# Kernel tuning notes

Measured on AMD Instinct MI355X. Metric: run time of the kernel, lower is better.

The kernel has to match this reference:

```python
import jax, jax.numpy as jnp
import numpy as np

DIM = 1024
NUM_HEADS = 16
HEAD_DIM = DIM // NUM_HEADS
WINDOW = 1024
GATE_IN = 20
B, T = 2, 2048
ROPE_BASE = 10000.0


def setup_inputs() -> dict:
    key = jax.random.key(0)
    ks = jax.random.split(key, 12)
    s = 0.02
    x = jax.random.normal(ks[0], (B, T, DIM), dtype=jnp.float32)
    Wq = jax.random.normal(ks[1], (DIM, DIM), dtype=jnp.float32) * s
    bq = jnp.zeros((DIM,), jnp.float32)
    Wk = jax.random.normal(ks[2], (DIM, DIM), dtype=jnp.float32) * s
    bk = jnp.zeros((DIM,), jnp.float32)
    Wv = jax.random.normal(ks[3], (DIM, DIM), dtype=jnp.float32) * s
    bv = jnp.zeros((DIM,), jnp.float32)
    # o_lin.weight is zero-initialized in the original; use random here so the
    # reference output/grads are non-degenerate.
    Wo = jax.random.normal(ks[4], (DIM, DIM), dtype=jnp.float32) * s
    bo = jnp.zeros((DIM,), jnp.float32)
    Wg = jax.random.normal(ks[5], (NUM_HEADS, GATE_IN), dtype=jnp.float32) * s
    bg = jnp.zeros((NUM_HEADS,), jnp.float32)
    # rotary tables, half-dim convention
    inv_freq = 1.0 / (ROPE_BASE ** (jnp.arange(0, HEAD_DIM, 2, dtype=jnp.float32) / HEAD_DIM))
    t = jnp.arange(T, dtype=jnp.float32)
    freqs = jnp.outer(t, inv_freq)  # [T, HEAD_DIM/2]
    return {"x": x, "Wq": Wq, "bq": bq, "Wk": Wk, "bk": bk, "Wv": Wv, "bv": bv,
            "Wo": Wo, "bo": bo, "Wg": Wg, "bg": bg,
            "cos": jnp.cos(freqs), "sin": jnp.sin(freqs)}


def _rope(u, cos, sin):
    # u: [B,T,H,hd]; cos/sin: [T, hd/2]
    u1, u2 = jnp.split(u, 2, axis=-1)
    c = cos[None, :, None, :]
    s = sin[None, :, None, :]
    return jnp.concatenate([u1 * c - u2 * s, u1 * s + u2 * c], axis=-1)


def reference(x, Wq, bq, Wk, bk, Wv, bv, Wo, bo, Wg, bg, cos, sin):
    Bx, Tx, D = x.shape
    q = (x @ Wq.T + bq).reshape(Bx, Tx, NUM_HEADS, HEAD_DIM)
    k = (x @ Wk.T + bk).reshape(Bx, Tx, NUM_HEADS, HEAD_DIM)
    v = (x @ Wv.T + bv).reshape(Bx, Tx, NUM_HEADS, HEAD_DIM)
    q = _rope(q, cos, sin)
    k = _rope(k, cos, sin)
    scale = 1.0 / jnp.sqrt(jnp.float32(HEAD_DIM))
    scores = jnp.einsum('bqhd,bkhd->bhqk', q, k) * scale  # [B,H,T,T]
    i = jnp.arange(Tx)[:, None]
    j = jnp.arange(Tx)[None, :]
    mask = (j <= i) & (j >= i - WINDOW)  # causal + sliding window (WINDOW left, 0 right)
    scores = jnp.where(mask[None, None], scores, jnp.float32(-1e30))
    probs = jax.nn.softmax(scores, axis=-1)
    o = jnp.einsum('bhqk,bkhd->bqhd', probs, v)  # [B,T,H,hd]
    gate = jax.nn.sigmoid(x[..., :GATE_IN] @ Wg.T + bg)  # [B,T,H]
    o = o * gate[..., None]
    o = o.reshape(Bx, Tx, D)
    return o @ Wo.T + bo
```

## Files before the change

kernel.cpp:

```cpp
#include <hip/hip_runtime.h>

#define DIMM 1024
#define NHEADS 16
#define HDIM 64
#define WIN 1024
#define GATEIN 20
#define BB 2
#define TT 2048
#define MTOT (BB*TT)

typedef __attribute__((ext_vector_type(8))) short short8;
typedef __attribute__((ext_vector_type(4))) float f32x4;
typedef __attribute__((ext_vector_type(16))) float f32x16;
typedef const __attribute__((address_space(1))) void gvoid_t;
typedef __attribute__((address_space(3))) void lvoid_t;

__device__ __forceinline__ unsigned short f2b(float f) {
  union { float f; unsigned u; } c; c.f = f;
  unsigned u = c.u + 0x7fffu + ((c.u >> 16) & 1u);
  return (unsigned short)(u >> 16);
}
__device__ __forceinline__ float b2f(unsigned short s) {
  union { unsigned u; float f; } c; c.u = ((unsigned)s) << 16;
  return c.f;
}
__device__ __forceinline__ unsigned cvt_pk_bf16(float lo, float hi) {
  unsigned r;
  asm("v_cvt_pk_bf16_f32 %0, %1, %2" : "=v"(r) : "v"(lo), "v"(hi));
  return r;
}
__device__ __forceinline__ float max3f(float a, float b, float c) {
  return fmaxf(fmaxf(a, b), c);
}
__device__ __forceinline__ float xmax32(float x) {
  union { float f; unsigned u; } c; c.f = x;
  auto pr = __builtin_amdgcn_permlane32_swap(c.u, c.u, false, false);
  union { unsigned u; float f; } a, b; a.u = pr[0]; b.u = pr[1];
  return fmaxf(a.f, b.f);
}
__device__ __forceinline__ float xsum32(float x) {
  union { float f; unsigned u; } c; c.f = x;
  auto pr = __builtin_amdgcn_permlane32_swap(c.u, c.u, false, false);
  union { unsigned u; float f; } a, b; a.u = pr[0]; b.u = pr[1];
  return a.f + b.f;
}

__global__ void prep_kernel(const float* __restrict__ x,  const float* __restrict__ Wq,
                            const float* __restrict__ Wk, const float* __restrict__ Wv,
                            const float* __restrict__ Wo, const float* __restrict__ bq,
                            const float* __restrict__ bk, const float* __restrict__ bv,
                            unsigned short* __restrict__ xb, unsigned short* __restrict__ wqkv,
                            unsigned short* __restrict__ wob, float* __restrict__ bcat) {
  int i = blockIdx.x * blockDim.x + threadIdx.x;
  const float* src; unsigned short* dst; int off;
  if (i < 1048576)      { src = x;  dst = xb;             off = i; }
  else if (i < 1310720) { src = Wq; dst = wqkv;           off = i - 1048576; }
  else if (i < 1572864) { src = Wk; dst = wqkv + 1048576; off = i - 1310720; }
  else if (i < 1835008) { src = Wv; dst = wqkv + 2097152; off = i - 1572864; }
  else if (i < 2097152) { src = Wo; dst = wob;            off = i - 1835008; }
  else {
    int j = i - 2097152;
    if (j < 768) {
      const float* bsrc = (j < 256) ? bq : (j < 512) ? bk : bv;
      int bo = (j & 255) * 4;
      int db = (j < 256) ? 0 : (j < 512) ? 1024 : 2048;
      *(float4*)(bcat + db + bo) = *(const float4*)(bsrc + bo);
    }
    return;
  }
  float4 v = ((const float4*)src)[off];
  union { unsigned short s[4]; uint2 u; } o;
  o.s[0] = f2b(v.x); o.s[1] = f2b(v.y); o.s[2] = f2b(v.z); o.s[3] = f2b(v.w);
  *(uint2*)(dst + (size_t)off * 4) = o.u;
}

__global__ void gate_kernel(const float* __restrict__ x, const float* __restrict__ Wg,
                            const float* __restrict__ bg, float* __restrict__ gate) {
  int i = blockIdx.x * blockDim.x + threadIdx.x;
  if (i >= MTOT * NHEADS) return;
  int h = i & 15;
  int m = i >> 4;
  const float* xr = x + (size_t)m * DIMM;
  const float* wr = Wg + h * GATEIN;
  float z = bg[h];
#pragma unroll
  for (int g = 0; g < GATEIN; ++g) z += xr[g] * wr[g];
  gate[i] = 1.f / (1.f + __expf(-z));
}

template<int MF, int OUTBF>
__global__ __launch_bounds__(256) void gemm_bt(const unsigned short* __restrict__ A,
                                               const unsigned short* __restrict__ Bw,
                                               const float* __restrict__ bias,
                                               void* __restrict__ Cout,
                                               int M, int N, int K) {
  __shared__ __align__(16) unsigned short As[2][MF * 32 * 32];
  __shared__ __align__(16) unsigned short Bs[2][128 * 32];
  const int tid = threadIdx.x;
  const int lane = tid & 63, wid = tid >> 6;
  const int g = lane >> 4, r16 = lane & 15;
  const int m0 = blockIdx.y * (MF * 32), n0 = blockIdx.x * 128;
  const int wr = (wid >> 1) * (MF * 16), wc = (wid & 1) * 64;
  const int wbase = wid * 64;

  int oaf[MF], obf[4];
#pragma unroll
  for (int mf = 0; mf < MF; ++mf) {
    int row = wr + mf * 16 + r16;
    oaf[mf] = row * 32 + ((g ^ ((row >> 1) & 3)) * 8);
  }
#pragma unroll
  for (int nf = 0; nf < 4; ++nf) {
    int row = wc + nf * 16 + r16;
    obf[nf] = row * 32 + ((g ^ ((row >> 1) & 3)) * 8);
  }

  f32x4 acc[MF][4];
#pragma unroll
  for (int i = 0; i < MF; ++i)
#pragma unroll
    for (int j = 0; j < 4; ++j) acc[i][j] = (f32x4){0.f, 0.f, 0.f, 0.f};

  auto stage = [&](int buf, int k0) {
#pragma unroll
    for (int j = 0; j < MF / 2; ++j) {
      int sbase = j * 256 + wbase;
      int s = sbase + lane;
      int l = s ^ ((s >> 3) & 3);
      const unsigned short* gA = A + (size_t)(m0 + (l >> 2)) * K + k0 + (l & 3) * 8;
      __builtin_amdgcn_global_load_lds((gvoid_t*)gA,
          (lvoid_t*)((char*)&As[buf][0] + sbase * 16), 16, 0, 0);
    }
#pragma unroll
    for (int j = 0; j < 2; ++j) {
      int sbase = j * 256 + wbase;
      int s = sbase + lane;
      int l = s ^ ((s >> 3) & 3);
      const unsigned short* gB = Bw + (size_t)(n0 + (l >> 2)) * K + k0 + (l & 3) * 8;
      __builtin_amdgcn_global_load_lds((gvoid_t*)gB,
          (lvoid_t*)((char*)&Bs[buf][0] + sbase * 16), 16, 0, 0);
    }
  };

  const int NT = K >> 5;
  stage(0, 0);
  __syncthreads();
  for (int t = 0; t < NT; ++t) {
    const int buf = t & 1;
    if (t + 1 < NT) stage(buf ^ 1, (t + 1) << 5);
    short8 af[MF], bf[4];
#pragma unroll
    for (int mf = 0; mf < MF; ++mf) af[mf] = *(const short8*)(&As[buf][0] + oaf[mf]);
#pragma unroll
    for (int nf = 0; nf < 4; ++nf)  bf[nf] = *(const short8*)(&Bs[buf][0] + obf[nf]);
#pragma unroll
    for (int mf = 0; mf < MF; ++mf)
#pragma unroll
      for (int nf = 0; nf < 4; ++nf)
        acc[mf][nf] = __builtin_amdgcn_mfma_f32_16x16x32_bf16(af[mf], bf[nf], acc[mf][nf], 0, 0, 0);
    __syncthreads();
  }
#pragma unroll
  for (int mf = 0; mf < MF; ++mf)
#pragma unroll
    for (int nf = 0; nf < 4; ++nf)
#pragma unroll
      for (int rr = 0; rr < 4; ++rr) {
        int m = m0 + wr + mf * 16 + g * 4 + rr;
        int n = n0 + wc + nf * 16 + r16;
        float v = acc[mf][nf][rr] + bias[n];
        if (OUTBF) ((unsigned short*)Cout)[(size_t)m * N + n] = f2b(v);
        else       ((float*)Cout)[(size_t)m * N + n] = v;
      }
}

#define QSCALE (0.125f * 1.4426950408889634f)
__global__ __launch_bounds__(256) void ropev_kernel(const unsigned short* __restrict__ qkv,
                                                    const float* __restrict__ cosb,
                                                    const float* __restrict__ sinb,
                                                    unsigned short* __restrict__ qr,
                                                    unsigned short* __restrict__ kr,
                                                    unsigned short* __restrict__ vt) {
  __shared__ unsigned short tile[64][66];
  const int t0 = blockIdx.x * 64;
  const int bh = blockIdx.y;
  const int b = bh >> 4, h = bh & 15;
  const int tid = threadIdx.x;
  const int tr = tid >> 2;
  const int qd = tid & 3;
  const int t = t0 + tr;
  const size_t base = (size_t)bh * TT * HDIM;
  const unsigned short* row = qkv + (size_t)(b * TT + t) * 3072 + h * 64;

  {
    const unsigned short* vsrc = row + 2048 + qd * 16;
    short8 v0 = *(const short8*)vsrc;
    short8 v1 = *(const short8*)(vsrc + 8);
#pragma unroll
    for (int j = 0; j < 8; ++j) {
      tile[tr][qd * 16 + j]     = (unsigned short)v0[j];
      tile[tr][qd * 16 + 8 + j] = (unsigned short)v1[j];
    }
  }

  {
    const int d0 = qd * 8;
    short8 q1 = *(const short8*)(row + d0);
    short8 q2 = *(const short8*)(row + d0 + 32);
    short8 k1 = *(const short8*)(row + 1024 + d0);
    short8 k2 = *(const short8*)(row + 1024 + d0 + 32);
    float4 c0 = *(const float4*)(cosb + t * 32 + d0);
    float4 c1 = *(const float4*)(cosb + t * 32 + d0 + 4);
    float4 s0 = *(const float4*)(sinb + t * 32 + d0);
    float4 s1 = *(const float4*)(sinb + t * 32 + d0 + 4);
    float cc[8] = {c0.x, c0.y, c0.z, c0.w, c1.x, c1.y, c1.z, c1.w};
    float ss[8] = {s0.x, s0.y, s0.z, s0.w, s1.x, s1.y, s1.z, s1.w};
    short8 qo1, qo2, ko1, ko2;
#pragma unroll
    for (int j = 0; j < 8; ++j) {
      float a1 = b2f((unsigned short)q1[j]), a2 = b2f((unsigned short)q2[j]);
      float b1 = b2f((unsigned short)k1[j]), b2v = b2f((unsigned short)k2[j]);
      qo1[j] = (short)f2b((a1 * cc[j] - a2 * ss[j]) * QSCALE);
      qo2[j] = (short)f2b((a1 * ss[j] + a2 * cc[j]) * QSCALE);
      ko1[j] = (short)f2b(b1 * cc[j] - b2v * ss[j]);
      ko2[j] = (short)f2b(b1 * ss[j] + b2v * cc[j]);
    }
    *(short8*)(qr + base + (size_t)t * HDIM + d0)      = qo1;
    *(short8*)(qr + base + (size_t)t * HDIM + d0 + 32) = qo2;
    size_t ok = base + (size_t)(t >> 5) * 2048 + (size_t)(qd >> 1) * 512
              + (size_t)(qd & 1) * 256 + (size_t)(t & 31) * 8;
    *(short8*)(kr + ok)        = ko1;
    *(short8*)(kr + ok + 1024) = ko2;
  }
  __syncthreads();

  {
    const int d = tid >> 2;
    const int tc = (tid & 3) * 16;
    short8 o0, o1;
#pragma unroll
    for (int j = 0; j < 8; ++j) {
      o0[j] = (short)tile[tc + j][d];
      o1[j] = (short)tile[tc + 8 + j][d];
    }
    int kt = (t0 + tc) >> 5;
    int n  = (tc >> 4) & 1;
    int m  = d >> 5, l31v = d & 31;
    size_t A0 = base + (size_t)kt * 2048 + (size_t)(m * 2 + n) * 512 + (size_t)l31v * 8;
    *(short8*)(vt + A0)       = o0;
    *(short8*)(vt + A0 + 256) = o1;
  }
}

__global__ __launch_bounds__(256, 4) void attn_kernel(const unsigned short* __restrict__ qr,
                                                      const unsigned short* __restrict__ kr,
                                                      const unsigned short* __restrict__ vt,
                                                      const float* __restrict__ gate,
                                                      unsigned short* __restrict__ attn_out) {
  __shared__ float lds_m[4][32];
  __shared__ float lds_l[4][32];
  __shared__ float lds_O[3][64][33];
  const int tid = threadIdx.x;
  const int lane = tid & 63, wid = tid >> 6;
  const int l31 = lane & 31, hi = lane >> 5;

  const int fid = blockIdx.x;
  const int idx = fid >> 3;
  const int bh = (fid & 7) * 4 + (idx & 3);
  const int qt = 63 - (idx >> 2);
  const int q0 = qt * 32;
  const int b = bh >> 4, h = bh & 15;
  const unsigned short* kptr = kr + (size_t)bh * TT * HDIM;
  const unsigned short* vptr = vt + (size_t)bh * TT * HDIM;
  const int q = q0 + l31;

  short8 qf[4];
#pragma unroll
  for (int st = 0; st < 4; ++st)
    qf[st] = *(const short8*)(qr + (size_t)bh * TT * HDIM + (size_t)q * HDIM + st * 16 + hi * 8);

  f32x16 o0, o1;
#pragma unroll
  for (int r = 0; r < 16; ++r) { o0[r] = 0.f; o1[r] = 0.f; }
  float mrun = -1e30f, lrun = 0.f;

  int kv_lo = q0 - WIN;
  if (kv_lo < 0) kv_lo = 0;
  const int kv_hi = q0 + 32;

  for (int kv = kv_lo + wid * 32; kv < kv_hi; kv += 128) {
    const unsigned short* kf = kptr + (size_t)kv * 64 + lane * 8;
    short8 k0 = *(const short8*)(kf);
    short8 k1 = *(const short8*)(kf + 512);
    short8 k2 = *(const short8*)(kf + 1024);
    short8 k3 = *(const short8*)(kf + 1536);

    f32x16 s;
#pragma unroll
    for (int r = 0; r < 16; ++r) s[r] = 0.f;
    s = __builtin_amdgcn_mfma_f32_32x32x16_bf16(k0, qf[0], s, 0, 0, 0);
    s = __builtin_amdgcn_mfma_f32_32x32x16_bf16(k1, qf[1], s, 0, 0, 0);
    s = __builtin_amdgcn_mfma_f32_32x32x16_bf16(k2, qf[2], s, 0, 0, 0);
    s = __builtin_amdgcn_mfma_f32_32x32x16_bf16(k3, qf[3], s, 0, 0, 0);

    if (kv == q0) {
#pragma unroll
      for (int r = 0; r < 16; ++r) {
        int key = kv + (r & 3) + 8 * (r >> 2) + 4 * hi;
        s[r] = (key <= q) ? s[r] : -1e30f;
      }
    } else if (q0 >= WIN && kv == kv_lo) {
#pragma unroll
      for (int r = 0; r < 16; ++r) {
        int key = kv + (r & 3) + 8 * (r >> 2) + 4 * hi;
        s[r] = (key + WIN >= q) ? s[r] : -1e30f;
      }
    }

    float t0 = max3f(s[0],  s[1],  s[2]);
    float t1 = max3f(s[3],  s[4],  s[5]);
    float t2 = max3f(s[6],  s[7],  s[8]);
    float t3 = max3f(s[9],  s[10], s[11]);
    float t4 = max3f(s[12], s[13], s[14]);
    float lm = fmaxf(max3f(t0, t1, t2), max3f(t3, t4, s[15]));
    lm = xmax32(lm);

    if (!__all(lm - mrun <= 8.f)) {
      float mnew = fmaxf(mrun, lm);
      float scf = __builtin_exp2f(mrun - mnew);
      mrun = mnew;
      lrun *= scf;
#pragma unroll
      for (int r = 0; r < 16; ++r) { o0[r] *= scf; o1[r] *= scf; }
    }

#pragma unroll
    for (int r = 0; r < 16; ++r) s[r] = __builtin_exp2f(s[r] - mrun);

    float c0 = (s[0] + s[1]) + (s[2] + s[3]);
    float c1 = (s[4] + s[5]) + (s[6] + s[7]);
    float c2 = (s[8] + s[9]) + (s[10] + s[11]);
    float c3 = (s[12] + s[13]) + (s[14] + s[15]);
    lrun += xsum32((c0 + c1) + (c2 + c3));

    unsigned w0 = cvt_pk_bf16(s[0],  s[1]),  w1 = cvt_pk_bf16(s[2],  s[3]);
    unsigned w2 = cvt_pk_bf16(s[4],  s[5]),  w3 = cvt_pk_bf16(s[6],  s[7]);
    unsigned w4 = cvt_pk_bf16(s[8],  s[9]),  w5 = cvt_pk_bf16(s[10], s[11]);
    unsigned w6 = cvt_pk_bf16(s[12], s[13]), w7 = cvt_pk_bf16(s[14], s[15]);
    auto s1p = __builtin_amdgcn_permlane32_swap(w0, w2, false, false);
    auto s2p = __builtin_amdgcn_permlane32_swap(w1, w3, false, false);
    auto s3p = __builtin_amdgcn_permlane32_swap(w4, w6, false, false);
    auto s4p = __builtin_amdgcn_permlane32_swap(w5, w7, false, false);
    union { unsigned u[4]; short8 s8; } pf0, pf1;
    pf0.u[0] = s1p[0]; pf0.u[1] = s2p[0]; pf0.u[2] = s1p[1]; pf0.u[3] = s2p[1];
    pf1.u[0] = s3p[0]; pf1.u[1] = s4p[0]; pf1.u[2] = s3p[1]; pf1.u[3] = s4p[1];

    const unsigned short* vf = vptr + (size_t)kv * 64 + lane * 8;
    short8 vf00 = *(const short8*)(vf);
    short8 vf01 = *(const short8*)(vf + 512);
    short8 vf10 = *(const short8*)(vf + 1024);
    short8 vf11 = *(const short8*)(vf + 1536);

    o0 = __builtin_amdgcn_mfma_f32_32x32x16_bf16(vf00, pf0.s8, o0, 0, 0, 0);
    o1 = __builtin_amdgcn_mfma_f32_32x32x16_bf16(vf10, pf0.s8, o1, 0, 0, 0);
    o0 = __builtin_amdgcn_mfma_f32_32x32x16_bf16(vf01, pf1.s8, o0, 0, 0, 0);
    o1 = __builtin_amdgcn_mfma_f32_32x32x16_bf16(vf11, pf1.s8, o1, 0, 0, 0);
  }

  if (hi == 0) { lds_m[wid][l31] = mrun; lds_l[wid][l31] = lrun; }
  __syncthreads();
  float m0 = lds_m[0][l31], m1 = lds_m[1][l31], m2 = lds_m[2][l31], m3 = lds_m[3][l31];
  float mstar = fmaxf(fmaxf(m0, m1), fmaxf(m2, m3));
  float myscale = __builtin_exp2f(mrun - mstar);
  if (wid != 0) {
#pragma unroll
    for (int r = 0; r < 16; ++r) {
      lds_O[wid - 1][lane][r]      = o0[r] * myscale;
      lds_O[wid - 1][lane][16 + r] = o1[r] * myscale;
    }
  }
  __syncthreads();
  if (wid == 0) {
    float lstar = __builtin_exp2f(m0 - mstar) * lds_l[0][l31]
                + __builtin_exp2f(m1 - mstar) * lds_l[1][l31]
                + __builtin_exp2f(m2 - mstar) * lds_l[2][l31]
                + __builtin_exp2f(m3 - mstar) * lds_l[3][l31];
    float gv = gate[((size_t)b * TT + q) * NHEADS + h];
    float inv = gv / lstar;
    float of0[16], of1[16];
#pragma unroll
    for (int r = 0; r < 16; ++r) {
      of0[r] = o0[r] * myscale + lds_O[0][lane][r]      + lds_O[1][lane][r]      + lds_O[2][lane][r];
      of1[r] = o1[r] * myscale + lds_O[0][lane][16 + r] + lds_O[1][lane][16 + r] + lds_O[2][lane][16 + r];
    }
    unsigned short* orow = attn_out + ((size_t)b * TT + q) * DIMM + h * HDIM;
#pragma unroll
    for (int a2 = 0; a2 < 4; ++a2) {
      int d0 = a2 * 8 + hi * 4;
      union { unsigned short s[4]; uint2 u; } x0, x1;
#pragma unroll
      for (int c = 0; c < 4; ++c) {
        x0.s[c] = f2b(of0[a2 * 4 + c] * inv);
        x1.s[c] = f2b(of1[a2 * 4 + c] * inv);
      }
      *(uint2*)(orow + d0) = x0.u;
      *(uint2*)(orow + 32 + d0) = x1.u;
    }
  }
}

#define OFF_XB    ((size_t)0)
#define OFF_WQKV  ((size_t)8388608)
#define OFF_WO    ((size_t)14680064)
#define OFF_BCAT  ((size_t)16777216)
#define OFF_QKV   ((size_t)16793600)
#define OFF_QR    ((size_t)41959424)
#define OFF_KR    ((size_t)50348032)
#define OFF_VT    ((size_t)58736640)
#define OFF_ATTN  ((size_t)67125248)
#define OFF_GATE  ((size_t)75513856)

extern "C" void kernel_launch(void* const* d_in, const int* in_sizes, int n_in,
                              void* d_out, int out_size, void* d_ws, size_t ws_size,
                              hipStream_t stream) {
  const float* x    = (const float*)d_in[0];
  const float* Wq   = (const float*)d_in[1];
  const float* bq   = (const float*)d_in[2];
  const float* Wk   = (const float*)d_in[3];
  const float* bk   = (const float*)d_in[4];
  const float* Wv   = (const float*)d_in[5];
  const float* bv   = (const float*)d_in[6];
  const float* Wo   = (const float*)d_in[7];
  const float* bo   = (const float*)d_in[8];
  const float* Wg   = (const float*)d_in[9];
  const float* bg   = (const float*)d_in[10];
  const float* cosb = (const float*)d_in[11];
  const float* sinb = (const float*)d_in[12];
  float* out = (float*)d_out;
  char* ws = (char*)d_ws;

  unsigned short* xb    = (unsigned short*)(ws + OFF_XB);
  unsigned short* wqkv  = (unsigned short*)(ws + OFF_WQKV);
  unsigned short* wob   = (unsigned short*)(ws + OFF_WO);
  float*          bcat  = (float*)(ws + OFF_BCAT);
  unsigned short* qkv   = (unsigned short*)(ws + OFF_QKV);
  unsigned short* q_r   = (unsigned short*)(ws + OFF_QR);
  unsigned short* k_r   = (unsigned short*)(ws + OFF_KR);
  unsigned short* v_t   = (unsigned short*)(ws + OFF_VT);
  unsigned short* attn  = (unsigned short*)(ws + OFF_ATTN);
  float*          gateb = (float*)(ws + OFF_GATE);

  prep_kernel<<<8195, 256, 0, stream>>>(x, Wq, Wk, Wv, Wo, bq, bk, bv, xb, wqkv, wob, bcat);
  gate_kernel<<<256, 256, 0, stream>>>(x, Wg, bg, gateb);

  gemm_bt<4, 1><<<dim3(24, 32), 256, 0, stream>>>(xb, wqkv, bcat, qkv, MTOT, 3072, 1024);

  ropev_kernel<<<dim3(32, 32), 256, 0, stream>>>(qkv, cosb, sinb, q_r, k_r, v_t);

  attn_kernel<<<2048, 256, 0, stream>>>(q_r, k_r, v_t, gateb, attn);

  gemm_bt<2, 0><<<dim3(8, 64), 256, 0, stream>>>(attn, wob, bo, out, MTOT, 1024, 1024);
}
```

Measured before the change: 107.4 us.

## Fuse RoPE, Q scaling and V transpose into the QKV GEMM epilogue

```diff
diff --git a/kernel.cpp b/kernel.cpp
--- a/kernel.cpp
+++ b/kernel.cpp
@@ -44,6 +44,8 @@
   union { unsigned u; float f; } a, b; a.u = pr[0]; b.u = pr[1];
   return a.f + b.f;
 }
+
+#define QSCALE (0.125f * 1.4426950408889634f)
 
 __global__ void prep_kernel(const float* __restrict__ x,  const float* __restrict__ Wq,
                             const float* __restrict__ Wk, const float* __restrict__ Wv,
@@ -88,11 +90,136 @@
   gate[i] = 1.f / (1.f + __expf(-z));
 }
 
-template<int MF, int OUTBF>
+__global__ __launch_bounds__(256) void gemm_qkv(const unsigned short* __restrict__ A,
+                                                const unsigned short* __restrict__ Bw,
+                                                const float* __restrict__ bias,
+                                                const float* __restrict__ cosb,
+                                                const float* __restrict__ sinb,
+                                                unsigned short* __restrict__ qr,
+                                                unsigned short* __restrict__ kr,
+                                                unsigned short* __restrict__ vt) {
+  const int M = MTOT, N = 3072, K = DIMM;
+  __shared__ __align__(16) unsigned short As[2][128 * 32];
+  __shared__ __align__(16) unsigned short Bs[2][128 * 32];
+  const int tid = threadIdx.x;
+  const int lane = tid & 63, wid = tid >> 6;
+  const int g = lane >> 4, r16 = lane & 15;
+  const int m0 = blockIdx.y * 128, n0 = blockIdx.x * 128;
+  const int wr = (wid >> 1) * 64, wc = (wid & 1) * 64;
+  const int wbase = wid * 64;
+
+  int oaf[4], obf[4];
+#pragma unroll
+  for (int mf = 0; mf < 4; ++mf) {
+    int row = wr + mf * 16 + r16;
+    oaf[mf] = row * 32 + ((g ^ ((row >> 1) & 3)) * 8);
+  }
+#pragma unroll
+  for (int nf = 0; nf < 4; ++nf) {
+    int row = wc + nf * 16 + r16;
+    obf[nf] = row * 32 + ((g ^ ((row >> 1) & 3)) * 8);
+  }
+
+  f32x4 acc[4][4];
+#pragma unroll
+  for (int i = 0; i < 4; ++i)
+#pragma unroll
+    for (int j = 0; j < 4; ++j) acc[i][j] = (f32x4){0.f, 0.f, 0.f, 0.f};
+
+  auto stage = [&](int buf, int k0) {
+#pragma unroll
+    for (int j = 0; j < 2; ++j) {
+      int sbase = j * 256 + wbase;
+      int s = sbase + lane;
+      int l = s ^ ((s >> 3) & 3);
+      const unsigned short* gA = A + (size_t)(m0 + (l >> 2)) * K + k0 + (l & 3) * 8;
+      __builtin_amdgcn_global_load_lds((gvoid_t*)gA,
+          (lvoid_t*)((char*)&As[buf][0] + sbase * 16), 16, 0, 0);
+      const unsigned short* gB = Bw + (size_t)(n0 + (l >> 2)) * K + k0 + (l & 3) * 8;
+      __builtin_amdgcn_global_load_lds((gvoid_t*)gB,
+          (lvoid_t*)((char*)&Bs[buf][0] + sbase * 16), 16, 0, 0);
+    }
+  };
+
+  const int NT = K >> 5;
+  stage(0, 0);
+  __syncthreads();
+  for (int t = 0; t < NT; ++t) {
+    const int buf = t & 1;
+    if (t + 1 < NT) stage(buf ^ 1, (t + 1) << 5);
+    short8 af[4], bf[4];
+#pragma unroll
+    for (int mf = 0; mf < 4; ++mf) af[mf] = *(const short8*)(&As[buf][0] + oaf[mf]);
+#pragma unroll
+    for (int nf = 0; nf < 4; ++nf)  bf[nf] = *(const short8*)(&Bs[buf][0] + obf[nf]);
+#pragma unroll
+    for (int mf = 0; mf < 4; ++mf)
+#pragma unroll
+      for (int nf = 0; nf < 4; ++nf)
+        acc[mf][nf] = __builtin_amdgcn_mfma_f32_16x16x32_bf16(af[mf], bf[nf], acc[mf][nf], 0, 0, 0);
+    __syncthreads();
+  }
+
+  const int ncol = n0 + wc;
+  const int seg  = ncol >> 10;
+  const int h    = (ncol >> 6) & 15;
+  const int bb   = m0 >> 11;
+  const int tb   = (m0 + wr) & 2047;
+  const size_t base = (size_t)(bb * NHEADS + h) * TT * HDIM;
+  float bias_v[4];
+#pragma unroll
+  for (int nf = 0; nf < 4; ++nf) bias_v[nf] = bias[ncol + nf * 16 + r16];
+
+  if (seg == 2) {
+#pragma unroll
+    for (int mf = 0; mf < 4; ++mf) {
+      int kvt = (tb >> 5) + (mf >> 1);
+#pragma unroll
+      for (int nf = 0; nf < 4; ++nf) {
+        union { unsigned short s4[4]; uint2 u; } w;
+#pragma unroll
+        for (int rr = 0; rr < 4; ++rr) w.s4[rr] = f2b(acc[mf][nf][rr] + bias_v[nf]);
+        size_t addr = base + (size_t)kvt * 2048
+                    + (size_t)((nf >> 1) * 2 + (mf & 1)) * 512
+                    + (size_t)(g >> 1) * 256
+                    + (size_t)((nf & 1) * 16 + r16) * 8 + 4 * (g & 1);
+        *(uint2*)(vt + addr) = w.u;
+      }
+    }
+  } else {
+#pragma unroll
+    for (int mf = 0; mf < 4; ++mf) {
+#pragma unroll
+      for (int rr = 0; rr < 4; ++rr) {
+        int t = tb + mf * 16 + g * 4 + rr;
+#pragma unroll
+        for (int nf = 0; nf < 2; ++nf) {
+          int d = nf * 16 + r16;
+          float c = cosb[t * 32 + d], s = sinb[t * 32 + d];
+          float v1 = acc[mf][nf][rr]     + bias_v[nf];
+          float v2 = acc[mf][nf + 2][rr] + bias_v[nf + 2];
+          float o1 = v1 * c - v2 * s;
+          float o2 = v1 * s + v2 * c;
+          if (seg == 0) {
+            qr[base + (size_t)t * HDIM + d]      = f2b(o1 * QSCALE);
+            qr[base + (size_t)t * HDIM + d + 32] = f2b(o2 * QSCALE);
+          } else {
+            size_t ok = base + (size_t)(t >> 5) * 2048 + (size_t)nf * 512
+                      + (size_t)(r16 >> 3) * 256 + (size_t)(t & 31) * 8 + (r16 & 7);
+            kr[ok]        = f2b(o1);
+            kr[ok + 1024] = f2b(o2);
+          }
+        }
+      }
+    }
+  }
+}
+
+template<int MF>
 __global__ __launch_bounds__(256) void gemm_bt(const unsigned short* __restrict__ A,
                                                const unsigned short* __restrict__ Bw,
                                                const float* __restrict__ bias,
-                                               void* __restrict__ Cout,
+                                               float* __restrict__ Cout,
                                                int M, int N, int K) {
   __shared__ __align__(16) unsigned short As[2][MF * 32 * 32];
   __shared__ __align__(16) unsigned short Bs[2][128 * 32];
@@ -168,88 +295,8 @@
       for (int rr = 0; rr < 4; ++rr) {
         int m = m0 + wr + mf * 16 + g * 4 + rr;
         int n = n0 + wc + nf * 16 + r16;
-        float v = acc[mf][nf][rr] + bias[n];
-        if (OUTBF) ((unsigned short*)Cout)[(size_t)m * N + n] = f2b(v);
-        else       ((float*)Cout)[(size_t)m * N + n] = v;
+        Cout[(size_t)m * N + n] = acc[mf][nf][rr] + bias[n];
       }
-}
-
-#define QSCALE (0.125f * 1.4426950408889634f)
-__global__ __launch_bounds__(256) void ropev_kernel(const unsigned short* __restrict__ qkv,
-                                                    const float* __restrict__ cosb,
-                                                    const float* __restrict__ sinb,
-                                                    unsigned short* __restrict__ qr,
-                                                    unsigned short* __restrict__ kr,
-                                                    unsigned short* __restrict__ vt) {
-  __shared__ unsigned short tile[64][66];
-  const int t0 = blockIdx.x * 64;
-  const int bh = blockIdx.y;
-  const int b = bh >> 4, h = bh & 15;
-  const int tid = threadIdx.x;
-  const int tr = tid >> 2;
-  const int qd = tid & 3;
-  const int t = t0 + tr;
-  const size_t base = (size_t)bh * TT * HDIM;
-  const unsigned short* row = qkv + (size_t)(b * TT + t) * 3072 + h * 64;
-
-  {
-    const unsigned short* vsrc = row + 2048 + qd * 16;
-    short8 v0 = *(const short8*)vsrc;
-    short8 v1 = *(const short8*)(vsrc + 8);
-#pragma unroll
-    for (int j = 0; j < 8; ++j) {
-      tile[tr][qd * 16 + j]     = (unsigned short)v0[j];
-      tile[tr][qd * 16 + 8 + j] = (unsigned short)v1[j];
-    }
-  }
-
-  {
-    const int d0 = qd * 8;
-    short8 q1 = *(const short8*)(row + d0);
-    short8 q2 = *(const short8*)(row + d0 + 32);
-    short8 k1 = *(const short8*)(row + 1024 + d0);
-    short8 k2 = *(const short8*)(row + 1024 + d0 + 32);
-    float4 c0 = *(const float4*)(cosb + t * 32 + d0);
-    float4 c1 = *(const float4*)(cosb + t * 32 + d0 + 4);
-    float4 s0 = *(const float4*)(sinb + t * 32 + d0);
-    float4 s1 = *(const float4*)(sinb + t * 32 + d0 + 4);
-    float cc[8] = {c0.x, c0.y, c0.z, c0.w, c1.x, c1.y, c1.z, c1.w};
-    float ss[8] = {s0.x, s0.y, s0.z, s0.w, s1.x, s1.y, s1.z, s1.w};
-    short8 qo1, qo2, ko1, ko2;
-#pragma unroll
-    for (int j = 0; j < 8; ++j) {
-      float a1 = b2f((unsigned short)q1[j]), a2 = b2f((unsigned short)q2[j]);
-      float b1 = b2f((unsigned short)k1[j]), b2v = b2f((unsigned short)k2[j]);
-      qo1[j] = (short)f2b((a1 * cc[j] - a2 * ss[j]) * QSCALE);
-      qo2[j] = (short)f2b((a1 * ss[j] + a2 * cc[j]) * QSCALE);
-      ko1[j] = (short)f2b(b1 * cc[j] - b2v * ss[j]);
-      ko2[j] = (short)f2b(b1 * ss[j] + b2v * cc[j]);
-    }
-    *(short8*)(qr + base + (size_t)t * HDIM + d0)      = qo1;
-    *(short8*)(qr + base + (size_t)t * HDIM + d0 + 32) = qo2;
-    size_t ok = base + (size_t)(t >> 5) * 2048 + (size_t)(qd >> 1) * 512
-              + (size_t)(qd & 1) * 256 + (size_t)(t & 31) * 8;
-    *(short8*)(kr + ok)        = ko1;
-    *(short8*)(kr + ok + 1024) = ko2;
-  }
-  __syncthreads();
-
-  {
-    const int d = tid >> 2;
-    const int tc = (tid & 3) * 16;
-    short8 o0, o1;
-#pragma unroll
-    for (int j = 0; j < 8; ++j) {
-      o0[j] = (short)tile[tc + j][d];
-      o1[j] = (short)tile[tc + 8 + j][d];
-    }
-    int kt = (t0 + tc) >> 5;
-    int n  = (tc >> 4) & 1;
-    int m  = d >> 5, l31v = d & 31;
-    size_t A0 = base + (size_t)kt * 2048 + (size_t)(m * 2 + n) * 512 + (size_t)l31v * 8;
-    *(short8*)(vt + A0)       = o0;
-    *(short8*)(vt + A0 + 256) = o1;
-  }
 }
 
 __global__ __launch_bounds__(256, 4) void attn_kernel(const unsigned short* __restrict__ qr,
@@ -413,7 +460,6 @@
 #define OFF_WQKV  ((size_t)8388608)
 #define OFF_WO    ((size_t)14680064)
 #define OFF_BCAT  ((size_t)16777216)
-#define OFF_QKV   ((size_t)16793600)
 #define OFF_QR    ((size_t)41959424)
 #define OFF_KR    ((size_t)50348032)
 #define OFF_VT    ((size_t)58736640)
@@ -443,7 +489,6 @@
   unsigned short* wqkv  = (unsigned short*)(ws + OFF_WQKV);
   unsigned short* wob   = (unsigned short*)(ws + OFF_WO);
   float*          bcat  = (float*)(ws + OFF_BCAT);
-  unsigned short* qkv   = (unsigned short*)(ws + OFF_QKV);
   unsigned short* q_r   = (unsigned short*)(ws + OFF_QR);
   unsigned short* k_r   = (unsigned short*)(ws + OFF_KR);
   unsigned short* v_t   = (unsigned short*)(ws + OFF_VT);
@@ -453,11 +498,9 @@
   prep_kernel<<<8195, 256, 0, stream>>>(x, Wq, Wk, Wv, Wo, bq, bk, bv, xb, wqkv, wob, bcat);
   gate_kernel<<<256, 256, 0, stream>>>(x, Wg, bg, gateb);
 
-  gemm_bt<4, 1><<<dim3(24, 32), 256, 0, stream>>>(xb, wqkv, bcat, qkv, MTOT, 3072, 1024);
-
-  ropev_kernel<<<dim3(32, 32), 256, 0, stream>>>(qkv, cosb, sinb, q_r, k_r, v_t);
+  gemm_qkv<<<dim3(24, 32), 256, 0, stream>>>(xb, wqkv, bcat, cosb, sinb, q_r, k_r, v_t);
 
   attn_kernel<<<2048, 256, 0, stream>>>(q_r, k_r, v_t, gateb, attn);
 
-  gemm_bt<2, 0><<<dim3(8, 64), 256, 0, stream>>>(attn, wob, bo, out, MTOT, 1024, 1024);
-}
+  gemm_bt<2><<<dim3(8, 64), 256, 0, stream>>>(attn, wob, bo, out, MTOT, 1024, 1024);
+}
```

Measured after the change: 106.6 us, median of 2. About the same (-0.8%).

## Replace QKV GEMM with 256x256-tile, 512-thread kernel and deeper prefetch

Applied to the files above, without the earlier changes.

```diff
diff --git a/kernel.cpp b/kernel.cpp
--- a/kernel.cpp
+++ b/kernel.cpp
@@ -44,6 +44,8 @@
   union { unsigned u; float f; } a, b; a.u = pr[0]; b.u = pr[1];
   return a.f + b.f;
 }
+
+#define QSCALE (0.125f * 1.4426950408889634f)
 
 __global__ void prep_kernel(const float* __restrict__ x,  const float* __restrict__ Wq,
                             const float* __restrict__ Wk, const float* __restrict__ Wv,
@@ -88,93 +90,98 @@
   gate[i] = 1.f / (1.f + __expf(-z));
 }
 
-template<int MF, int OUTBF>
-__global__ __launch_bounds__(256) void gemm_bt(const unsigned short* __restrict__ A,
-                                               const unsigned short* __restrict__ Bw,
-                                               const float* __restrict__ bias,
-                                               void* __restrict__ Cout,
-                                               int M, int N, int K) {
-  __shared__ __align__(16) unsigned short As[2][MF * 32 * 32];
-  __shared__ __align__(16) unsigned short Bs[2][128 * 32];
+__global__ __launch_bounds__(512, 2) void gemm_qkv_256(const unsigned short* __restrict__ A,
+                                                       const unsigned short* __restrict__ Bw,
+                                                       const float* __restrict__ bias,
+                                                       unsigned short* __restrict__ qkv) {
+  const int K = DIMM, N = 3072;
+  __shared__ __align__(16) unsigned short ldsA[2][16384];
+  __shared__ __align__(16) unsigned short ldsB[2][16384];
   const int tid = threadIdx.x;
   const int lane = tid & 63, wid = tid >> 6;
   const int g = lane >> 4, r16 = lane & 15;
-  const int m0 = blockIdx.y * (MF * 32), n0 = blockIdx.x * 128;
-  const int wr = (wid >> 1) * (MF * 16), wc = (wid & 1) * 64;
-  const int wbase = wid * 64;
-
-  int oaf[MF], obf[4];
-#pragma unroll
-  for (int mf = 0; mf < MF; ++mf) {
-    int row = wr + mf * 16 + r16;
-    oaf[mf] = row * 32 + ((g ^ ((row >> 1) & 3)) * 8);
-  }
-#pragma unroll
-  for (int nf = 0; nf < 4; ++nf) {
-    int row = wc + nf * 16 + r16;
-    obf[nf] = row * 32 + ((g ^ ((row >> 1) & 3)) * 8);
-  }
-
-  f32x4 acc[MF][4];
-#pragma unroll
-  for (int i = 0; i < MF; ++i)
+  const int wm = wid >> 2, wn = wid & 3;
+  const int m0 = blockIdx.y * 256, n0 = blockIdx.x * 256;
+
+  int aoff[8][2], boff[4][2];
+#pragma unroll
+  for (int fr = 0; fr < 8; ++fr)
+#pragma unroll
+    for (int ks = 0; ks < 2; ++ks) {
+      int lb = (wm * 128 + fr * 16 + r16) * 128 + ks * 64 + g * 16;
+      aoff[fr][ks] = lb ^ (((lb >> 9) & 1) << 5);
+    }
+#pragma unroll
+  for (int fc = 0; fc < 4; ++fc)
+#pragma unroll
+    for (int ks = 0; ks < 2; ++ks) {
+      int lb = (wn * 64 + fc * 16 + r16) * 128 + ks * 64 + g * 16;
+      boff[fc][ks] = lb ^ (((lb >> 9) & 1) << 5);
+    }
+
+  f32x4 acc[8][4];
+#pragma unroll
+  for (int i = 0; i < 8; ++i)
 #pragma unroll
     for (int j = 0; j < 4; ++j) acc[i][j] = (f32x4){0.f, 0.f, 0.f, 0.f};
 
-  auto stage = [&](int buf, int k0) {
-#pragma unroll
-    for (int j = 0; j < MF / 2; ++j) {
-      int sbase = j * 256 + wbase;
-      int s = sbase + lane;
-      int l = s ^ ((s >> 3) & 3);
-      const unsigned short* gA = A + (size_t)(m0 + (l >> 2)) * K + k0 + (l & 3) * 8;
+  auto stage = [&](int buf, int kt) {
+    const int k0 = kt * 64;
+#pragma unroll
+    for (int i = 0; i < 4; ++i) {
+      int s = i * 512 + tid;
+      int l = s ^ (((s >> 5) & 1) << 1);
+      const unsigned short* gA = A + (size_t)(m0 + (l >> 3)) * K + k0 + (l & 7) * 8;
       __builtin_amdgcn_global_load_lds((gvoid_t*)gA,
-          (lvoid_t*)((char*)&As[buf][0] + sbase * 16), 16, 0, 0);
-    }
-#pragma unroll
-    for (int j = 0; j < 2; ++j) {
-      int sbase = j * 256 + wbase;
-      int s = sbase + lane;
-      int l = s ^ ((s >> 3) & 3);
-      const unsigned short* gB = Bw + (size_t)(n0 + (l >> 2)) * K + k0 + (l & 3) * 8;
+          (lvoid_t*)((char*)&ldsA[buf][0] + s * 16), 16, 0, 0);
+      const unsigned short* gB = Bw + (size_t)(n0 + (l >> 3)) * K + k0 + (l & 7) * 8;
       __builtin_amdgcn_global_load_lds((gvoid_t*)gB,
-          (lvoid_t*)((char*)&Bs[buf][0] + sbase * 16), 16, 0, 0);
+          (lvoid_t*)((char*)&ldsB[buf][0] + s * 16), 16, 0, 0);
     }
   };
 
-  const int NT = K >> 5;
+  const int NT = K >> 6;
   stage(0, 0);
-  __syncthreads();
+  stage(1, 1);
   for (int t = 0; t < NT; ++t) {
     const int buf = t & 1;
-    if (t + 1 < NT) stage(buf ^ 1, (t + 1) << 5);
-    short8 af[MF], bf[4];
-#pragma unroll
-    for (int mf = 0; mf < MF; ++mf) af[mf] = *(const short8*)(&As[buf][0] + oaf[mf]);
-#pragma unroll
-    for (int nf = 0; nf < 4; ++nf)  bf[nf] = *(const short8*)(&Bs[buf][0] + obf[nf]);
-#pragma unroll
-    for (int mf = 0; mf < MF; ++mf)
-#pragma unroll
-      for (int nf = 0; nf < 4; ++nf)
-        acc[mf][nf] = __builtin_amdgcn_mfma_f32_16x16x32_bf16(af[mf], bf[nf], acc[mf][nf], 0, 0, 0);
-    __syncthreads();
-  }
-#pragma unroll
-  for (int mf = 0; mf < MF; ++mf)
-#pragma unroll
-    for (int nf = 0; nf < 4; ++nf)
+    if (t < NT - 1) asm volatile("s_waitcnt vmcnt(8)" ::: "memory");
+    else            asm volatile("s_waitcnt vmcnt(0)" ::: "memory");
+    __builtin_amdgcn_s_barrier();
+
+    const char* Ab = (const char*)&ldsA[buf][0];
+    const char* Bb = (const char*)&ldsB[buf][0];
+    __builtin_amdgcn_s_setprio(1);
+#pragma unroll
+    for (int ks = 0; ks < 2; ++ks) {
+      short8 af[8], bf[4];
+#pragma unroll
+      for (int fr = 0; fr < 8; ++fr) af[fr] = *(const short8*)(Ab + aoff[fr][ks]);
+#pragma unroll
+      for (int fc = 0; fc < 4; ++fc) bf[fc] = *(const short8*)(Bb + boff[fc][ks]);
+#pragma unroll
+      for (int fr = 0; fr < 8; ++fr)
+#pragma unroll
+        for (int fc = 0; fc < 4; ++fc)
+          acc[fr][fc] = __builtin_amdgcn_mfma_f32_16x16x32_bf16(af[fr], bf[fc], acc[fr][fc], 0, 0, 0);
+    }
+    __builtin_amdgcn_s_setprio(0);
+    __builtin_amdgcn_s_barrier();
+    if (t + 2 < NT) stage(buf, t + 2);
+  }
+
+#pragma unroll
+  for (int fr = 0; fr < 8; ++fr)
+#pragma unroll
+    for (int fc = 0; fc < 4; ++fc)
 #pragma unroll
       for (int rr = 0; rr < 4; ++rr) {
-        int m = m0 + wr + mf * 16 + g * 4 + rr;
-        int n = n0 + wc + nf * 16 + r16;
-        float v = acc[mf][nf][rr] + bias[n];
-        if (OUTBF) ((unsigned short*)Cout)[(size_t)m * N + n] = f2b(v);
-        else       ((float*)Cout)[(size_t)m * N + n] = v;
+        int m = m0 + wm * 128 + fr * 16 + g * 4 + rr;
+        int n = n0 + wn * 64 + fc * 16 + r16;
+        qkv[(size_t)m * N + n] = f2b(acc[fr][fc][rr] + bias[n]);
       }
 }
 
-#define QSCALE (0.125f * 1.4426950408889634f)
 __global__ __launch_bounds__(256) void ropev_kernel(const unsigned short* __restrict__ qkv,
                                                     const float* __restrict__ cosb,
                                                     const float* __restrict__ sinb,
@@ -250,6 +257,90 @@
     *(short8*)(vt + A0)       = o0;
     *(short8*)(vt + A0 + 256) = o1;
   }
+}
+
+template<int MF>
+__global__ __launch_bounds__(256) void gemm_bt(const unsigned short* __restrict__ A,
+                                               const unsigned short* __restrict__ Bw,
+                                               const float* __restrict__ bias,
+                                               float* __restrict__ Cout,
+                                               int M, int N, int K) {
+  __shared__ __align__(16) unsigned short As[2][MF * 32 * 32];
+  __shared__ __align__(16) unsigned short Bs[2][128 * 32];
+  const int tid = threadIdx.x;
+  const int lane = tid & 63, wid = tid >> 6;
+  const int g = lane >> 4, r16 = lane & 15;
+  const int m0 = blockIdx.y * (MF * 32), n0 = blockIdx.x * 128;
+  const int wr = (wid >> 1) * (MF * 16), wc = (wid & 1) * 64;
+  const int wbase = wid * 64;
+
+  int oaf[MF], obf[4];
+#pragma unroll
+  for (int mf = 0; mf < MF; ++mf) {
+    int row = wr + mf * 16 + r16;
+    oaf[mf] = row * 32 + ((g ^ ((row >> 1) & 3)) * 8);
+  }
+#pragma unroll
+  for (int nf = 0; nf < 4; ++nf) {
+    int row = wc + nf * 16 + r16;
+    obf[nf] = row * 32 + ((g ^ ((row >> 1) & 3)) * 8);
+  }
+
+  f32x4 acc[MF][4];
+#pragma unroll
+  for (int i = 0; i < MF; ++i)
+#pragma unroll
+    for (int j = 0; j < 4; ++j) acc[i][j] = (f32x4){0.f, 0.f, 0.f, 0.f};
+
+  auto stage = [&](int buf, int k0) {
+#pragma unroll
+    for (int j = 0; j < MF / 2; ++j) {
+      int sbase = j * 256 + wbase;
+      int s = sbase + lane;
+      int l = s ^ ((s >> 3) & 3);
+      const unsigned short* gA = A + (size_t)(m0 + (l >> 2)) * K + k0 + (l & 3) * 8;
+      __builtin_amdgcn_global_load_lds((gvoid_t*)gA,
+          (lvoid_t*)((char*)&As[buf][0] + sbase * 16), 16, 0, 0);
+    }
+#pragma unroll
+    for (int j = 0; j < 2; ++j) {
+      int sbase = j * 256 + wbase;
+      int s = sbase + lane;
+      int l = s ^ ((s >> 3) & 3);
+      const unsigned short* gB = Bw + (size_t)(n0 + (l >> 2)) * K + k0 + (l & 3) * 8;
+      __builtin_amdgcn_global_load_lds((gvoid_t*)gB,
+          (lvoid_t*)((char*)&Bs[buf][0] + sbase * 16), 16, 0, 0);
+    }
+  };
+
+  const int NT = K >> 5;
+  stage(0, 0);
+  __syncthreads();
+  for (int t = 0; t < NT; ++t) {
+    const int buf = t & 1;
+    if (t + 1 < NT) stage(buf ^ 1, (t + 1) << 5);
+    short8 af[MF], bf[4];
+#pragma unroll
+    for (int mf = 0; mf < MF; ++mf) af[mf] = *(const short8*)(&As[buf][0] + oaf[mf]);
+#pragma unroll
+    for (int nf = 0; nf < 4; ++nf)  bf[nf] = *(const short8*)(&Bs[buf][0] + obf[nf]);
+#pragma unroll
+    for (int mf = 0; mf < MF; ++mf)
+#pragma unroll
+      for (int nf = 0; nf < 4; ++nf)
+        acc[mf][nf] = __builtin_amdgcn_mfma_f32_16x16x32_bf16(af[mf], bf[nf], acc[mf][nf], 0, 0, 0);
+    __syncthreads();
+  }
+#pragma unroll
+  for (int mf = 0; mf < MF; ++mf)
+#pragma unroll
+    for (int nf = 0; nf < 4; ++nf)
+#pragma unroll
+      for (int rr = 0; rr < 4; ++rr) {
+        int m = m0 + wr + mf * 16 + g * 4 + rr;
+        int n = n0 + wc + nf * 16 + r16;
+        Cout[(size_t)m * N + n] = acc[mf][nf][rr] + bias[n];
+      }
 }
 
 __global__ __launch_bounds__(256, 4) void attn_kernel(const unsigned short* __restrict__ qr,
@@ -453,11 +544,11 @@
   prep_kernel<<<8195, 256, 0, stream>>>(x, Wq, Wk, Wv, Wo, bq, bk, bv, xb, wqkv, wob, bcat);
   gate_kernel<<<256, 256, 0, stream>>>(x, Wg, bg, gateb);
 
-  gemm_bt<4, 1><<<dim3(24, 32), 256, 0, stream>>>(xb, wqkv, bcat, qkv, MTOT, 3072, 1024);
+  gemm_qkv_256<<<dim3(12, 16), 512, 0, stream>>>(xb, wqkv, bcat, qkv);
 
   ropev_kernel<<<dim3(32, 32), 256, 0, stream>>>(qkv, cosb, sinb, q_r, k_r, v_t);
 
   attn_kernel<<<2048, 256, 0, stream>>>(q_r, k_r, v_t, gateb, attn);
 
-  gemm_bt<2, 0><<<dim3(8, 64), 256, 0, stream>>>(attn, wob, bo, out, MTOT, 1024, 1024);
-}
+  gemm_bt<2><<<dim3(8, 64), 256, 0, stream>>>(attn, wob, bo, out, MTOT, 1024, 1024);
+}
```

Result: slower. 111.5 us (+3.8%).
